# Optimization experiments

Measured on AMD Instinct MI355X. Metric: run time of the kernel, lower is better.

Reference implementation:

```python
import jax, jax.numpy as jnp
import numpy as np

N = 50000      # nodes
E = 800000     # edges (before self-loops)
IN = 128
OUT = 128
HID = 2 * OUT  # hi=2 in the module
NEG_SLOPE = 0.2


def setup_inputs() -> dict:
    key = jax.random.key(0)
    ks = jax.random.split(key, 12)
    glorot = lambda k, shape: jax.random.normal(k, shape, jnp.float32) * (2.0 / (shape[0] + shape[-1])) ** 0.5
    return {
        "x": jax.random.normal(ks[0], (N, IN), jnp.float32),
        "edge_index": jax.random.randint(ks[1], (2, E), 0, N, jnp.int64),
        # layer 1: in -> 2*out
        "W1": glorot(ks[2], (IN, HID)),
        "a1_src": glorot(ks[3], (HID,)),
        "a1_dst": glorot(ks[4], (HID,)),
        "b1": jnp.zeros((HID,), jnp.float32),
        # layer 2: 2*out -> out
        "W2": glorot(ks[5], (HID, OUT)),
        "a2_src": glorot(ks[6], (OUT,)),
        "a2_dst": glorot(ks[7], (OUT,)),
        "b2": jnp.zeros((OUT,), jnp.float32),
    }


def gat_layer(x, src, dst, W, a_src, a_dst, b, n):
    # h = W x   [N, F]
    h = x @ W
    alpha_src = h @ a_src  # [N]
    alpha_dst = h @ a_dst  # [N]
    # per-edge attention logit, edge j->i uses src score of j + dst score of i
    e = jax.nn.leaky_relu(alpha_src[src] + alpha_dst[dst], NEG_SLOPE)  # [E']
    # numerically stable segment softmax over incoming edges of each dst node
    e_max = jax.lax.stop_gradient(jax.ops.segment_max(e, dst, num_segments=n))
    p = jnp.exp(e - e_max[dst])
    denom = jax.ops.segment_sum(p, dst, num_segments=n)
    alpha = p / (denom[dst] + 1e-16)  # [E']
    # weighted scatter-aggregate of source features
    out = jax.ops.segment_sum(h[src] * alpha[:, None], dst, num_segments=n)
    return out + b


def reference(x, edge_index, W1, a1_src, a1_dst, b1, W2, a2_src, a2_dst, b2):
    n = x.shape[0]
    loops = jnp.arange(n, dtype=edge_index.dtype)
    src = jnp.concatenate([edge_index[0], loops])  # add self-loops (PyG default)
    dst = jnp.concatenate([edge_index[1], loops])
    h = jax.nn.relu(gat_layer(x, src, dst, W1, a1_src, a1_dst, b1, n))
    out = jax.nn.relu(gat_layer(h, src, dst, W2, a2_src, a2_dst, b2, n))
    return out
```

## Files before the change

kernel.cpp:

```cpp
#include <hip/hip_runtime.h>
#include <hip/hip_bf16.h>
#include <float.h>
#include <stdint.h>

#define NEG_SLOPE 0.2f

typedef __attribute__((ext_vector_type(8))) short short8;
typedef __attribute__((ext_vector_type(4))) float f32x4;

#define BSTRIDE 3072

__device__ inline float b2f(unsigned short u) {
  return __uint_as_float((unsigned int)u << 16);
}
__device__ inline unsigned short f2b(float f) {
  unsigned int u = __float_as_uint(f);
  return (unsigned short)((u + 0x7FFF + ((u >> 16) & 1)) >> 16);
}
__device__ inline float leaky(float e) { return e >= 0.f ? e : NEG_SLOPE * e; }
__device__ inline float blo(unsigned int w) {
  return __uint_as_float(w << 16);
}
__device__ inline float bhi(unsigned int w) {
  return __uint_as_float(w & 0xFFFF0000u);
}

__device__ inline int load_idx(const void* ei, long long pos, int is64) {
  if (is64) return (int)((const long long*)ei)[pos];
  return ((const int*)ei)[pos];
}

__global__ __launch_bounds__(256) void prep_all(
    const float* __restrict__ W1, const float* __restrict__ W2,
    const float* __restrict__ a1s, const float* __restrict__ a1d,
    const float* __restrict__ a2s, const float* __restrict__ a2d,
    unsigned short* __restrict__ Wp1, unsigned short* __restrict__ Wp2,
    float* __restrict__ wa, int* __restrict__ bcur, const void* __restrict__ ei,
    int* __restrict__ flag64) {
  int b = blockIdx.x;
  int t = threadIdx.x;
  if (b < 128) {
    int i = b * 256 + t;
    int k = i >> 8, n = i & 255;
    Wp1[(((k >> 3) * 256 + n) << 3) + (k & 7)] = f2b(W1[i]);
  } else if (b < 256) {
    int i = (b - 128) * 256 + t;
    int k = i >> 7, n = i & 127;
    Wp2[(((k >> 3) * 128 + n) << 3) + (k & 7)] = f2b(W2[i]);
  } else if (b < 259) {
    int o = (b - 256) * 256 + t;
    float s = 0.f;
    if (o < 128) {
      for (int n = 0; n < 256; ++n) s += W1[o * 256 + n] * a1s[n];
    } else if (o < 256) {
      int k = o - 128;
      for (int n = 0; n < 256; ++n) s += W1[k * 256 + n] * a1d[n];
    } else if (o < 512) {
      int k = o - 256;
      for (int n = 0; n < 128; ++n) s += W2[k * 128 + n] * a2s[n];
    } else {
      int k = o - 512;
      for (int n = 0; n < 128; ++n) s += W2[k * 128 + n] * a2d[n];
    }
    wa[o] = s;
  } else {
    bcur[t] = 0;
    bcur[t + 256] = 0;
    if (t < 64) {
      const int* p = (const int*)ei;
      unsigned long long bl = __ballot(p[2 * t + 1] != 0);
      if (t == 0) *flag64 = (bl == 0ull) ? 1 : 0;
    }
  }
}

__global__ __launch_bounds__(256) void bin_edges(
    const void* __restrict__ ei, const int* __restrict__ flag64, int E,
    int* __restrict__ bcursor, unsigned int* __restrict__ binned) {
  __shared__ int hist[512];
  __shared__ int scn[512];
  __shared__ int gb[512];
  __shared__ unsigned int stage[2048];
  int t = threadIdx.x;
  hist[t] = 0; hist[t + 256] = 0;
  __syncthreads();
  const int is64 = *flag64;
  const long long base = (long long)blockIdx.x * 2048;
  const int cblk = (int)min((long long)2048, (long long)E - base);
  int sv[8];
  short bk[8], rk[8];
#pragma unroll
  for (int i = 0; i < 8; ++i) {
    int k = t + i * 256;
    if (k < cblk) {
      long long j = base + k;
      int s = load_idx(ei, j, is64);
      int d = load_idx(ei, (long long)E + j, is64);
      int b = d >> 7;
      bk[i] = (short)b;
      sv[i] = (s << 7) | (d & 127);
      rk[i] = (short)atomicAdd(&hist[b], 1);
    } else {
      bk[i] = -1;
    }
  }
  __syncthreads();
  scn[t] = hist[t]; scn[t + 256] = hist[t + 256];
  __syncthreads();
  for (int off = 1; off < 512; off <<= 1) {
    int v0 = (t >= off) ? scn[t - off] : 0;
    int v1 = scn[t + 256 - off];
    __syncthreads();
    scn[t] += v0;
    scn[t + 256] += v1;
    __syncthreads();
  }
  int c0 = hist[t], c1 = hist[t + 256];
  int l0 = scn[t] - c0, l1 = scn[t + 256] - c1;
  if (c0) gb[t] = atomicAdd(&bcursor[t], c0);
  if (c1) gb[t + 256] = atomicAdd(&bcursor[t + 256], c1);
  scn[t] = l0; scn[t + 256] = l1;
  __syncthreads();
#pragma unroll
  for (int i = 0; i < 8; ++i) {
    if (bk[i] >= 0)
      stage[scn[bk[i]] + rk[i]] = ((unsigned)(int)bk[i] << 23) | (unsigned)sv[i];
  }
  __syncthreads();
#pragma unroll
  for (int i = 0; i < 8; ++i) {
    int k = t + i * 256;
    if (k < cblk) {
      unsigned w = stage[k];
      int b = w >> 23;
      binned[(long long)b * BSTRIDE + gb[b] + (k - scn[b])] = w;
    }
  }
}

__global__ __launch_bounds__(256) void place_csr(
    const unsigned int* __restrict__ binned, const int* __restrict__ bcursor,
    int2* __restrict__ rowbe, unsigned short* __restrict__ csr, int Nn) {
  __shared__ int cnt[128], deg0[128], cur[128];
  int t = threadIdx.x;
  int b = blockIdx.x;
  if (t < 128) cnt[t] = 0;
  __syncthreads();
  const int rbeg = b * BSTRIDE;
  const int rend = rbeg + bcursor[b];
  for (int k = rbeg + t; k < rend; k += 256)
    atomicAdd(&cnt[binned[k] & 127], 1);
  __syncthreads();
  if (t < 128) deg0[t] = cnt[t];
  __syncthreads();
  for (int off = 1; off < 128; off <<= 1) {
    int v = (t >= off && t < 128) ? cnt[t - off] : 0;
    __syncthreads();
    if (t < 128) cnt[t] += v;
    __syncthreads();
  }
  const int node0 = b << 7;
  if (t < 128) {
    int start = rbeg + cnt[t] - deg0[t];
    int node = node0 + t;
    if (node < Nn) rowbe[node] = make_int2(start, start + deg0[t]);
    cur[t] = start;
  }
  __syncthreads();
  for (int k = rbeg + t; k < rend; k += 256) {
    unsigned w = binned[k];
    int pos = atomicAdd(&cur[w & 127], 1);
    csr[pos] = (unsigned short)((w >> 7) & 0xFFFF);
  }
}

__global__ __launch_bounds__(256) void alpha1_cast(
    const float* __restrict__ x, const float* __restrict__ wa,
    unsigned short* __restrict__ xb, float* __restrict__ as_out,
    float* __restrict__ ad_out, int Nn) {
  int node = blockIdx.x * 4 + (threadIdx.x >> 6);
  int lane = threadIdx.x & 63;
  if (node >= Nn) return;
  float2 v = *(const float2*)(x + (long long)node * 128 + lane * 2);
  float s1 = v.x * wa[lane * 2] + v.y * wa[lane * 2 + 1];
  float s2 = v.x * wa[128 + lane * 2] + v.y * wa[128 + lane * 2 + 1];
  unsigned int packed = (unsigned int)f2b(v.x) | ((unsigned int)f2b(v.y) << 16);
  *(unsigned int*)(xb + (long long)node * 128 + lane * 2) = packed;
#pragma unroll
  for (int off = 32; off > 0; off >>= 1) {
    s1 += __shfl_down(s1, off);
    s2 += __shfl_down(s2, off);
  }
  if (lane == 0) {
    as_out[node] = s1;
    ad_out[node] = s2;
  }
}

template <int Nn, int Kk, bool BIAS_RELU, bool SCORES>
__global__ __launch_bounds__(256) void gemm_mfma(
    const unsigned short* __restrict__ A, const unsigned short* __restrict__ Bp,
    unsigned short* __restrict__ C, int M, const float* __restrict__ bias,
    const float* __restrict__ was, const float* __restrict__ wad,
    float* __restrict__ s_as, float* __restrict__ s_ad) {
  const int l = threadIdx.x & 63;
  const int wm = threadIdx.x >> 6;
  const int bm = blockIdx.x * 64;
  const int bn = blockIdx.y * 64;
  const int arow = bm + wm * 16 + (l & 15);
  const int kg = l >> 4;

  f32x4 acc[4];
#pragma unroll
  for (int nt = 0; nt < 4; ++nt) acc[nt] = (f32x4){0.f, 0.f, 0.f, 0.f};

  const bool arow_ok = (arow < M);
  const bool do_scores = SCORES && (blockIdx.y == 0);
  float ps = 0.f, pd = 0.f;
#pragma unroll
  for (int kk = 0; kk < Kk; kk += 32) {
    short8 afrag;
    if (arow_ok)
      afrag = *(const short8*)(A + (long long)arow * Kk + kk + kg * 8);
    else
      afrag = (short8){0, 0, 0, 0, 0, 0, 0, 0};
    if (SCORES) {
      if (do_scores) {
        const int kb0 = kk + kg * 8;
#pragma unroll
        for (int i = 0; i < 8; ++i) {
          float v = b2f((unsigned short)afrag[i]);
          ps += v * was[kb0 + i];
          pd += v * wad[kb0 + i];
        }
      }
    }
    const int kb = (kk >> 3) + kg;
#pragma unroll
    for (int nt = 0; nt < 4; ++nt) {
      short8 bfrag = *(const short8*)(Bp + (((long long)kb * Nn + bn + nt * 16 +
                                             (l & 15))
                                            << 3));
      acc[nt] = __builtin_amdgcn_mfma_f32_16x16x32_bf16(afrag, bfrag, acc[nt],
                                                        0, 0, 0);
    }
  }
  if (SCORES) {
    if (do_scores) {
      ps += __shfl_xor(ps, 16); ps += __shfl_xor(ps, 32);
      pd += __shfl_xor(pd, 16); pd += __shfl_xor(pd, 32);
      if (l < 16 && arow_ok) {
        s_as[arow] = ps;
        s_ad[arow] = pd;
      }
    }
  }
#pragma unroll
  for (int nt = 0; nt < 4; ++nt) {
    const int col = bn + nt * 16 + (l & 15);
    float bv = BIAS_RELU ? bias[col] : 0.f;
#pragma unroll
    for (int r = 0; r < 4; ++r) {
      const int row = bm + wm * 16 + (l >> 4) * 4 + r;
      if (row < M) {
        float v = acc[nt][r];
        if (BIAS_RELU) v = fmaxf(v + bv, 0.f);
        C[(long long)row * Nn + col] = f2b(v);
      }
    }
  }
}

template <bool BIAS_RELU, bool OUT_BF16>
__global__ __launch_bounds__(256) void gat_aggregate(
    const int2* __restrict__ rowbe, const unsigned short* __restrict__ csr,
    const float* __restrict__ as, const float* __restrict__ ad,
    const unsigned short* __restrict__ h, const float* __restrict__ bias,
    void* __restrict__ outp, int Nn) {
  constexpr int F = 128;
  const int node = blockIdx.x * 16 + (threadIdx.x >> 4);
  const int hl = threadIdx.x & 15;
  if (node >= Nn) return;
  const int2 be = rowbe[node];
  int t = be.x;
  const int end = be.y;
  const float adn = ad[node];
  const int f0 = hl * 8;

  float m = leaky(as[node] + adn);
  float sg = 1.f;
  float acc[8];
  {
    uint4 w = *(const uint4*)(h + (long long)node * F + f0);
    acc[0] = blo(w.x); acc[1] = bhi(w.x);
    acc[2] = blo(w.y); acc[3] = bhi(w.y);
    acc[4] = blo(w.z); acc[5] = bhi(w.z);
    acc[6] = blo(w.w); acc[7] = bhi(w.w);
  }

  for (; t + 4 <= end; t += 4) {
    int s0 = csr[t], s1 = csr[t + 1], s2 = csr[t + 2], s3 = csr[t + 3];
    uint4 w0 = *(const uint4*)(h + (long long)s0 * F + f0);
    uint4 w1 = *(const uint4*)(h + (long long)s1 * F + f0);
    uint4 w2 = *(const uint4*)(h + (long long)s2 * F + f0);
    uint4 w3 = *(const uint4*)(h + (long long)s3 * F + f0);
    float e0 = leaky(as[s0] + adn);
    float e1 = leaky(as[s1] + adn);
    float e2 = leaky(as[s2] + adn);
    float e3 = leaky(as[s3] + adn);
    float em = fmaxf(fmaxf(e0, e1), fmaxf(e2, e3));
    if (em > m + 8.f) {
      float sc = __expf(m - em);
      sg *= sc;
#pragma unroll
      for (int j = 0; j < 8; ++j) acc[j] *= sc;
      m = em;
    }
    float p0 = __expf(e0 - m), p1 = __expf(e1 - m);
    float p2 = __expf(e2 - m), p3 = __expf(e3 - m);
    sg += (p0 + p1) + (p2 + p3);
    acc[0] += p0 * blo(w0.x) + p1 * blo(w1.x) + p2 * blo(w2.x) + p3 * blo(w3.x);
    acc[1] += p0 * bhi(w0.x) + p1 * bhi(w1.x) + p2 * bhi(w2.x) + p3 * bhi(w3.x);
    acc[2] += p0 * blo(w0.y) + p1 * blo(w1.y) + p2 * blo(w2.y) + p3 * blo(w3.y);
    acc[3] += p0 * bhi(w0.y) + p1 * bhi(w1.y) + p2 * bhi(w2.y) + p3 * bhi(w3.y);
    acc[4] += p0 * blo(w0.z) + p1 * blo(w1.z) + p2 * blo(w2.z) + p3 * blo(w3.z);
    acc[5] += p0 * bhi(w0.z) + p1 * bhi(w1.z) + p2 * bhi(w2.z) + p3 * bhi(w3.z);
    acc[6] += p0 * blo(w0.w) + p1 * blo(w1.w) + p2 * blo(w2.w) + p3 * blo(w3.w);
    acc[7] += p0 * bhi(w0.w) + p1 * bhi(w1.w) + p2 * bhi(w2.w) + p3 * bhi(w3.w);
  }
  for (; t < end; ++t) {
    int s = csr[t];
    uint4 w = *(const uint4*)(h + (long long)s * F + f0);
    float e = leaky(as[s] + adn);
    if (e > m + 8.f) {
      float sc = __expf(m - e);
      sg *= sc;
#pragma unroll
      for (int j = 0; j < 8; ++j) acc[j] *= sc;
      m = e;
    }
    float p = __expf(e - m);
    sg += p;
    acc[0] += p * blo(w.x); acc[1] += p * bhi(w.x);
    acc[2] += p * blo(w.y); acc[3] += p * bhi(w.y);
    acc[4] += p * blo(w.z); acc[5] += p * bhi(w.z);
    acc[6] += p * blo(w.w); acc[7] += p * bhi(w.w);
  }

  const float inv = 1.f / (sg + 1e-16f);
#pragma unroll
  for (int j = 0; j < 8; ++j) {
    acc[j] *= inv;
    if (BIAS_RELU) acc[j] = fmaxf(acc[j] + bias[f0 + j], 0.f);
  }
  if (OUT_BF16) {
    short8 o;
#pragma unroll
    for (int j = 0; j < 8; ++j) o[j] = (short)f2b(acc[j]);
    *(short8*)((unsigned short*)outp + (long long)node * F + f0) = o;
  } else {
    float4 o0 = {acc[0], acc[1], acc[2], acc[3]};
    float4 o1 = {acc[4], acc[5], acc[6], acc[7]};
    float* orow = (float*)outp + (long long)node * F + f0;
    *(float4*)(orow) = o0;
    *(float4*)(orow + 4) = o1;
  }
}

extern "C" void kernel_launch(void* const* d_in, const int* in_sizes, int n_in,
                              void* d_out, int out_size, void* d_ws,
                              size_t ws_size, hipStream_t stream) {
  const float* x      = (const float*)d_in[0];
  const void*  ei     = d_in[1];
  const float* W1     = (const float*)d_in[2];
  const float* a1_src = (const float*)d_in[3];
  const float* a1_dst = (const float*)d_in[4];
  const float* b1     = (const float*)d_in[5];
  const float* W2     = (const float*)d_in[6];
  const float* a2_src = (const float*)d_in[7];
  const float* a2_dst = (const float*)d_in[8];
  const float* b2     = (const float*)d_in[9];
  float* out = (float*)d_out;

  const int N = 50000, E = 800000, IN = 128, HID = 256, OUT = 128;
  const int NBLK_E = (E + 2047) / 2048;
  const int NB = (N + 127) >> 7;

  char* ws = (char*)d_ws;
  size_t off = 0;
  auto carve = [&](size_t bytes) -> void* {
    void* p = ws + off;
    off = (off + bytes + 255) & ~(size_t)255;
    return p;
  };
  unsigned short* xb     = (unsigned short*)carve((size_t)N * IN * 2);
  unsigned short* aggx   = (unsigned short*)carve((size_t)N * IN * 2);
  unsigned short* out1   = (unsigned short*)carve((size_t)N * HID * 2);
  unsigned short* h2     = (unsigned short*)carve((size_t)N * OUT * 2);
  unsigned short* Wp1    = (unsigned short*)carve((size_t)IN * HID * 2);
  unsigned short* Wp2    = (unsigned short*)carve((size_t)HID * OUT * 2);
  float*          wa     = (float*)carve(768 * 4);
  unsigned int*   binned = (unsigned int*)carve((size_t)NB * BSTRIDE * 4);
  unsigned short* csr    = (unsigned short*)carve((size_t)NB * BSTRIDE * 2);
  int*            bcur   = (int*)carve(512 * 4);
  int2*           rowbe  = (int2*)carve((size_t)N * 8);
  float*          as_    = (float*)carve((size_t)N * 4);
  float*          ad_    = (float*)carve((size_t)N * 4);
  float*          as2_   = (float*)carve((size_t)N * 4);
  float*          ad2_   = (float*)carve((size_t)N * 4);
  int*            flag64 = (int*)carve(256);
  (void)ws_size; (void)in_sizes; (void)n_in; (void)out_size;

  prep_all<<<260, 256, 0, stream>>>(W1, W2, a1_src, a1_dst, a2_src, a2_dst,
                                    Wp1, Wp2, wa, bcur, ei, flag64);

  bin_edges<<<NBLK_E, 256, 0, stream>>>(ei, flag64, E, bcur, binned);
  place_csr<<<NB, 256, 0, stream>>>(binned, bcur, rowbe, csr, N);

  const int nb4 = (N + 3) / 4;
  const int nb16 = (N + 15) / 16;

  alpha1_cast<<<nb4, 256, 0, stream>>>(x, wa, xb, as_, ad_, N);
  gat_aggregate<false, true><<<nb16, 256, 0, stream>>>(rowbe, csr, as_, ad_,
                                                       xb, nullptr, aggx, N);
  {
    dim3 g((N + 63) / 64, HID / 64);
    gemm_mfma<HID, IN, true, false><<<g, 256, 0, stream>>>(
        aggx, Wp1, out1, N, b1, nullptr, nullptr, nullptr, nullptr);
  }

  {
    dim3 g((N + 63) / 64, OUT / 64);
    gemm_mfma<OUT, HID, false, true><<<g, 256, 0, stream>>>(
        out1, Wp2, h2, N, nullptr, wa + 256, wa + 512, as2_, ad2_);
  }
  gat_aggregate<true, false><<<nb16, 256, 0, stream>>>(rowbe, csr, as2_,
                                                       ad2_, h2, b2, out, N);
}
```

Measured before the change: 154.7 us.

## Pad CSR rows to 8, vectorize index loads, fuse alpha cast into binning

Each CSR row is padded to a multiple of 8 entries and the padding is zero-filled, so the aggregation loop can load 8 source indices with one 16-byte read and process 8 neighbours per iteration, including a masked tail. The per-node alpha/cast work now runs as extra blocks of the edge-binning kernel, which removes one kernel launch and lets the two independent jobs overlap. The bin stride grows to hold the padding. The cost is more gather work on padded slots and higher register pressure from 8-wide unrolling.

```diff
diff --git a/kernel.cpp b/kernel.cpp
--- a/kernel.cpp
+++ b/kernel.cpp
@@ -8,7 +8,7 @@
 typedef __attribute__((ext_vector_type(8))) short short8;
 typedef __attribute__((ext_vector_type(4))) float f32x4;
 
-#define BSTRIDE 3072
+#define BSTRIDE 3584
 
 __device__ inline float b2f(unsigned short u) {
   return __uint_as_float((unsigned int)u << 16);
@@ -74,14 +74,38 @@
   }
 }
 
-__global__ __launch_bounds__(256) void bin_edges(
+__global__ __launch_bounds__(256) void bin_and_alpha(
     const void* __restrict__ ei, const int* __restrict__ flag64, int E,
-    int* __restrict__ bcursor, unsigned int* __restrict__ binned) {
+    int* __restrict__ bcursor, unsigned int* __restrict__ binned, int nblk,
+    const float* __restrict__ x, const float* __restrict__ wa,
+    unsigned short* __restrict__ xb, float* __restrict__ as_out,
+    float* __restrict__ ad_out, int Nn) {
   __shared__ int hist[512];
   __shared__ int scn[512];
   __shared__ int gb[512];
   __shared__ unsigned int stage[2048];
   int t = threadIdx.x;
+  if (blockIdx.x >= nblk) {
+    int node = (blockIdx.x - nblk) * 4 + (t >> 6);
+    int lane = t & 63;
+    if (node >= Nn) return;
+    float2 v = *(const float2*)(x + (long long)node * 128 + lane * 2);
+    float s1 = v.x * wa[lane * 2] + v.y * wa[lane * 2 + 1];
+    float s2 = v.x * wa[128 + lane * 2] + v.y * wa[128 + lane * 2 + 1];
+    unsigned int packed =
+        (unsigned int)f2b(v.x) | ((unsigned int)f2b(v.y) << 16);
+    *(unsigned int*)(xb + (long long)node * 128 + lane * 2) = packed;
+#pragma unroll
+    for (int off = 32; off > 0; off >>= 1) {
+      s1 += __shfl_down(s1, off);
+      s2 += __shfl_down(s2, off);
+    }
+    if (lane == 0) {
+      as_out[node] = s1;
+      ad_out[node] = s2;
+    }
+    return;
+  }
   hist[t] = 0; hist[t + 256] = 0;
   __syncthreads();
   const int is64 = *flag64;
@@ -141,7 +165,7 @@
 __global__ __launch_bounds__(256) void place_csr(
     const unsigned int* __restrict__ binned, const int* __restrict__ bcursor,
     int2* __restrict__ rowbe, unsigned short* __restrict__ csr, int Nn) {
-  __shared__ int cnt[128], deg0[128], cur[128];
+  __shared__ int cnt[128], deg0[128], cur[128], alc[128];
   int t = threadIdx.x;
   int b = blockIdx.x;
   if (t < 128) cnt[t] = 0;
@@ -151,7 +175,11 @@
   for (int k = rbeg + t; k < rend; k += 256)
     atomicAdd(&cnt[binned[k] & 127], 1);
   __syncthreads();
-  if (t < 128) deg0[t] = cnt[t];
+  if (t < 128) {
+    deg0[t] = cnt[t];
+    alc[t] = (cnt[t] + 7) & ~7;
+    cnt[t] = alc[t];
+  }
   __syncthreads();
   for (int off = 1; off < 128; off <<= 1) {
     int v = (t >= off && t < 128) ? cnt[t - off] : 0;
@@ -161,7 +189,7 @@
   }
   const int node0 = b << 7;
   if (t < 128) {
-    int start = rbeg + cnt[t] - deg0[t];
+    int start = rbeg + cnt[t] - alc[t];
     int node = node0 + t;
     if (node < Nn) rowbe[node] = make_int2(start, start + deg0[t]);
     cur[t] = start;
@@ -172,28 +200,11 @@
     int pos = atomicAdd(&cur[w & 127], 1);
     csr[pos] = (unsigned short)((w >> 7) & 0xFFFF);
   }
-}
-
-__global__ __launch_bounds__(256) void alpha1_cast(
-    const float* __restrict__ x, const float* __restrict__ wa,
-    unsigned short* __restrict__ xb, float* __restrict__ as_out,
-    float* __restrict__ ad_out, int Nn) {
-  int node = blockIdx.x * 4 + (threadIdx.x >> 6);
-  int lane = threadIdx.x & 63;
-  if (node >= Nn) return;
-  float2 v = *(const float2*)(x + (long long)node * 128 + lane * 2);
-  float s1 = v.x * wa[lane * 2] + v.y * wa[lane * 2 + 1];
-  float s2 = v.x * wa[128 + lane * 2] + v.y * wa[128 + lane * 2 + 1];
-  unsigned int packed = (unsigned int)f2b(v.x) | ((unsigned int)f2b(v.y) << 16);
-  *(unsigned int*)(xb + (long long)node * 128 + lane * 2) = packed;
-#pragma unroll
-  for (int off = 32; off > 0; off >>= 1) {
-    s1 += __shfl_down(s1, off);
-    s2 += __shfl_down(s2, off);
-  }
-  if (lane == 0) {
-    as_out[node] = s1;
-    ad_out[node] = s2;
+  __syncthreads();
+  if (t < 128 && (node0 + t) < Nn) {
+    int s0 = cur[t];
+    int s1 = rbeg + cnt[t];
+    for (int k = s0; k < s1; ++k) csr[k] = 0;
   }
 }
 
@@ -282,8 +293,7 @@
   const int hl = threadIdx.x & 15;
   if (node >= Nn) return;
   const int2 be = rowbe[node];
-  int t = be.x;
-  const int end = be.y;
+  const int beg = be.x, end = be.y;
   const float adn = ad[node];
   const int f0 = hl * 8;
 
@@ -298,17 +308,24 @@
     acc[6] = blo(w.w); acc[7] = bhi(w.w);
   }
 
-  for (; t + 4 <= end; t += 4) {
-    int s0 = csr[t], s1 = csr[t + 1], s2 = csr[t + 2], s3 = csr[t + 3];
-    uint4 w0 = *(const uint4*)(h + (long long)s0 * F + f0);
-    uint4 w1 = *(const uint4*)(h + (long long)s1 * F + f0);
-    uint4 w2 = *(const uint4*)(h + (long long)s2 * F + f0);
-    uint4 w3 = *(const uint4*)(h + (long long)s3 * F + f0);
-    float e0 = leaky(as[s0] + adn);
-    float e1 = leaky(as[s1] + adn);
-    float e2 = leaky(as[s2] + adn);
-    float e3 = leaky(as[s3] + adn);
-    float em = fmaxf(fmaxf(e0, e1), fmaxf(e2, e3));
+  int t = beg;
+  for (; t + 8 <= end; t += 8) {
+    uint4 c = *(const uint4*)(csr + t);
+    int s[8];
+    s[0] = c.x & 0xFFFF; s[1] = c.x >> 16;
+    s[2] = c.y & 0xFFFF; s[3] = c.y >> 16;
+    s[4] = c.z & 0xFFFF; s[5] = c.z >> 16;
+    s[6] = c.w & 0xFFFF; s[7] = c.w >> 16;
+    uint4 w[8];
+#pragma unroll
+    for (int i = 0; i < 8; ++i)
+      w[i] = *(const uint4*)(h + (long long)s[i] * F + f0);
+    float e[8];
+#pragma unroll
+    for (int i = 0; i < 8; ++i) e[i] = leaky(as[s[i]] + adn);
+    float em = e[0];
+#pragma unroll
+    for (int i = 1; i < 8; ++i) em = fmaxf(em, e[i]);
     if (em > m + 8.f) {
       float sc = __expf(m - em);
       sg *= sc;
@@ -316,35 +333,56 @@
       for (int j = 0; j < 8; ++j) acc[j] *= sc;
       m = em;
     }
-    float p0 = __expf(e0 - m), p1 = __expf(e1 - m);
-    float p2 = __expf(e2 - m), p3 = __expf(e3 - m);
-    sg += (p0 + p1) + (p2 + p3);
-    acc[0] += p0 * blo(w0.x) + p1 * blo(w1.x) + p2 * blo(w2.x) + p3 * blo(w3.x);
-    acc[1] += p0 * bhi(w0.x) + p1 * bhi(w1.x) + p2 * bhi(w2.x) + p3 * bhi(w3.x);
-    acc[2] += p0 * blo(w0.y) + p1 * blo(w1.y) + p2 * blo(w2.y) + p3 * blo(w3.y);
-    acc[3] += p0 * bhi(w0.y) + p1 * bhi(w1.y) + p2 * bhi(w2.y) + p3 * bhi(w3.y);
-    acc[4] += p0 * blo(w0.z) + p1 * blo(w1.z) + p2 * blo(w2.z) + p3 * blo(w3.z);
-    acc[5] += p0 * bhi(w0.z) + p1 * bhi(w1.z) + p2 * bhi(w2.z) + p3 * bhi(w3.z);
-    acc[6] += p0 * blo(w0.w) + p1 * blo(w1.w) + p2 * blo(w2.w) + p3 * blo(w3.w);
-    acc[7] += p0 * bhi(w0.w) + p1 * bhi(w1.w) + p2 * bhi(w2.w) + p3 * bhi(w3.w);
-  }
-  for (; t < end; ++t) {
-    int s = csr[t];
-    uint4 w = *(const uint4*)(h + (long long)s * F + f0);
-    float e = leaky(as[s] + adn);
-    if (e > m + 8.f) {
-      float sc = __expf(m - e);
+    float p[8];
+#pragma unroll
+    for (int i = 0; i < 8; ++i) p[i] = __expf(e[i] - m);
+#pragma unroll
+    for (int i = 0; i < 8; ++i) sg += p[i];
+#pragma unroll
+    for (int i = 0; i < 8; ++i) {
+      acc[0] += p[i] * blo(w[i].x); acc[1] += p[i] * bhi(w[i].x);
+      acc[2] += p[i] * blo(w[i].y); acc[3] += p[i] * bhi(w[i].y);
+      acc[4] += p[i] * blo(w[i].z); acc[5] += p[i] * bhi(w[i].z);
+      acc[6] += p[i] * blo(w[i].w); acc[7] += p[i] * bhi(w[i].w);
+    }
+  }
+  if (t < end) {
+    uint4 c = *(const uint4*)(csr + t);
+    int s[8];
+    s[0] = c.x & 0xFFFF; s[1] = c.x >> 16;
+    s[2] = c.y & 0xFFFF; s[3] = c.y >> 16;
+    s[4] = c.z & 0xFFFF; s[5] = c.z >> 16;
+    s[6] = c.w & 0xFFFF; s[7] = c.w >> 16;
+    uint4 w[8];
+#pragma unroll
+    for (int i = 0; i < 8; ++i)
+      w[i] = *(const uint4*)(h + (long long)s[i] * F + f0);
+    float e[8];
+#pragma unroll
+    for (int i = 0; i < 8; ++i)
+      e[i] = (t + i < end) ? leaky(as[s[i]] + adn) : -3.4e38f;
+    float em = e[0];
+#pragma unroll
+    for (int i = 1; i < 8; ++i) em = fmaxf(em, e[i]);
+    if (em > m + 8.f) {
+      float sc = __expf(m - em);
       sg *= sc;
 #pragma unroll
       for (int j = 0; j < 8; ++j) acc[j] *= sc;
-      m = e;
-    }
-    float p = __expf(e - m);
-    sg += p;
-    acc[0] += p * blo(w.x); acc[1] += p * bhi(w.x);
-    acc[2] += p * blo(w.y); acc[3] += p * bhi(w.y);
-    acc[4] += p * blo(w.z); acc[5] += p * bhi(w.z);
-    acc[6] += p * blo(w.w); acc[7] += p * bhi(w.w);
+      m = em;
+    }
+    float p[8];
+#pragma unroll
+    for (int i = 0; i < 8; ++i) p[i] = __expf(e[i] - m);
+#pragma unroll
+    for (int i = 0; i < 8; ++i) sg += p[i];
+#pragma unroll
+    for (int i = 0; i < 8; ++i) {
+      acc[0] += p[i] * blo(w[i].x); acc[1] += p[i] * bhi(w[i].x);
+      acc[2] += p[i] * blo(w[i].y); acc[3] += p[i] * bhi(w[i].y);
+      acc[4] += p[i] * blo(w[i].z); acc[5] += p[i] * bhi(w[i].z);
+      acc[6] += p[i] * blo(w[i].w); acc[7] += p[i] * bhi(w[i].w);
+    }
   }
 
   const float inv = 1.f / (sg + 1e-16f);
@@ -385,6 +423,8 @@
   const int N = 50000, E = 800000, IN = 128, HID = 256, OUT = 128;
   const int NBLK_E = (E + 2047) / 2048;
   const int NB = (N + 127) >> 7;
+  const int nb4 = (N + 3) / 4;
+  const int nb16 = (N + 15) / 16;
 
   char* ws = (char*)d_ws;
   size_t off = 0;
@@ -414,13 +454,11 @@
   prep_all<<<260, 256, 0, stream>>>(W1, W2, a1_src, a1_dst, a2_src, a2_dst,
                                     Wp1, Wp2, wa, bcur, ei, flag64);
 
-  bin_edges<<<NBLK_E, 256, 0, stream>>>(ei, flag64, E, bcur, binned);
+  bin_and_alpha<<<NBLK_E + nb4, 256, 0, stream>>>(
+      ei, flag64, E, bcur, binned, NBLK_E, x, wa, xb, as_, ad_, N);
+
   place_csr<<<NB, 256, 0, stream>>>(binned, bcur, rowbe, csr, N);
 
-  const int nb4 = (N + 3) / 4;
-  const int nb16 = (N + 15) / 16;
-
-  alpha1_cast<<<nb4, 256, 0, stream>>>(x, wa, xb, as_, ad_, N);
   gat_aggregate<false, true><<<nb16, 256, 0, stream>>>(rowbe, csr, as_, ad_,
                                                        xb, nullptr, aggx, N);
   {
```

New measurement: 151.2 us. -2.3%, faster.
